# Performance work log

Hardware: AMD Instinct MI355X
Metric: run time of the kernel (lower is better)

Reference implementation:

```python
import jax, jax.numpy as jnp
import numpy as np
from functools import partial

MASK_THRESH = 0.4
SCORE_THRESH = 0.35
SUPPRESS_IOU = 0.85
TOPK_KEEP = 40


def _logit(p):
    p = jnp.clip(p, 1e-4, 1.0 - 1e-4)
    return jnp.log(p) - jnp.log1p(-p)


def _greedy_keep(binm_f, labels, scores):
    # binm_f: [N, HW] float 0/1 masks, rows already sorted by descending score.
    # Precompute the pairwise mask-IoU matrix once (batched, memory-bound),
    # then run the sequential greedy suppression over the small NxN matrix.
    N = binm_f.shape[0]
    inter = binm_f @ binm_f.T                              # [N, N]
    area = jnp.sum(binm_f, axis=1)
    union = jnp.maximum(area[:, None] + area[None, :] - inter, 1.0)
    iou = inter / union
    conflict = (labels[:, None] == labels[None, :]) & (iou >= SUPPRESS_IOU)

    def body(i, state):
        kept, count, stopped = state
        stopped = stopped | (scores[i] < SCORE_THRESH)     # break on low score
        clash = jnp.any(kept & conflict[i])                # same-class high-IoU vs kept
        take = (~stopped) & (~clash)
        kept = kept.at[i].set(take)
        count = count + take.astype(jnp.int32)
        stopped = stopped | (count >= TOPK_KEEP)           # break after topk kept
        return kept, count, stopped

    kept0 = jnp.zeros((N,), dtype=bool)
    kept, count, _ = jax.lax.fori_loop(0, N, body, (kept0, jnp.int32(0), jnp.array(False)))
    return kept, count


def _per_image(masks, labels, scores, feat, class_count):
    N, H, W = masks.shape
    D, fh, fw = feat.shape
    order = jnp.argsort(-scores)
    masks = masks[order]
    labels = labels[order]
    scores = scores[order]
    binm = masks > MASK_THRESH
    kept, count = _greedy_keep(binm.reshape(N, -1).astype(masks.dtype), labels, scores)

    # pack kept entries into the leading slots, preserving score order
    key = jnp.where(kept, jnp.arange(N), N + jnp.arange(N))
    perm = jnp.argsort(key)
    masks_p = jnp.clip(masks[perm], 0.0, 1.0)
    labels_p = jnp.clip(labels[perm], 0, class_count - 1)
    scores_p = jnp.clip(scores[perm], 0.0, 1.0)
    valid = jnp.arange(N) < count                          # [Q], Q == N == max_queries

    mask_logits = jnp.where(valid[:, None, None], _logit(masks_p), -20.0)

    C1 = class_count + 1
    base = jnp.full((N, C1), -10.0, dtype=masks.dtype)     # default row (all -10)
    row = base.at[:, -1].set(0.0)                          # no-object col -> 0
    onehot = jax.nn.one_hot(labels_p, C1, dtype=masks.dtype)
    row = row + onehot * (_logit(scores_p)[:, None] + 10.0)
    class_logits = jnp.where(valid[:, None], row, base)

    binm_p = masks_p > MASK_THRESH
    xs = jnp.arange(W, dtype=masks.dtype)
    ys = jnp.arange(H, dtype=masks.dtype)
    big = jnp.asarray(1e9, masks.dtype)
    x1 = jnp.min(jnp.where(binm_p, xs[None, None, :], big), axis=(1, 2))
    x2 = jnp.max(jnp.where(binm_p, xs[None, None, :], -big), axis=(1, 2))
    y1 = jnp.min(jnp.where(binm_p, ys[None, :, None], big), axis=(1, 2))
    y2 = jnp.max(jnp.where(binm_p, ys[None, :, None], -big), axis=(1, 2))
    cx = (x1 + x2) * 0.5 / W
    cy = (y1 + y2) * 0.5 / H
    bw = jnp.maximum(x2 - x1, 0.0) / W
    bh = jnp.maximum(y2 - y1, 0.0) / H
    box = jnp.clip(jnp.stack([cx, cy, bw, bh], axis=-1), 0.0, 1.0)
    has_px = jnp.any(binm_p, axis=(1, 2))
    boxes = jnp.where((valid & has_px)[:, None], box, 0.0)

    # mask-pooled DINO embeddings (bilinear downsample == F.interpolate align_corners=False)
    mask_small = jax.image.resize(masks_p, (N, fh, fw), method='linear')
    denom = jnp.maximum(jnp.sum(mask_small, axis=(1, 2)), 1e-6)
    pooled = jnp.einsum('qhw,dhw->qd', mask_small, feat) / denom[:, None]
    norm = jnp.maximum(jnp.linalg.norm(pooled, axis=-1, keepdims=True), 1e-12)
    embs = jnp.where(valid[:, None], pooled / norm, 0.0)
    return mask_logits, class_logits, boxes, embs


def reference(masks, labels, scores, dino_feat_map, class_count):
    fn = lambda m, l, s, f: _per_image(m, l, s, f, class_count)
    return jax.vmap(fn)(masks, labels, scores, dino_feat_map)


def setup_inputs():
    key = jax.random.key(0)
    k1, k2, k3, k4 = jax.random.split(key, 4)
    B, N, H, W = 2, 100, 640, 640
    D, fh, fw = 384, 40, 40
    return {
        'masks': jax.random.uniform(k1, (B, N, H, W), dtype=jnp.float32),
        'labels': jax.random.randint(k2, (B, N), 0, 80),
        'scores': jax.random.uniform(k3, (B, N), dtype=jnp.float32),
        'dino_feat_map': jax.random.normal(k4, (B, D, fh, fw), dtype=jnp.float32),
        'class_count': 80,
    }
```

## Files before the change

### kernel.cpp

```cpp
#include <hip/hip_runtime.h>
#include <cstdint>
#include <climits>

constexpr int kB = 2;
constexpr int kN = 100;
constexpr int kH = 640;
constexpr int kW = 640;
constexpr int kHW = kH * kW;
constexpr int kWORDS = kHW / 64;
constexpr int kD = 384;
constexpr int kFH = 40;
constexpr int kFW = 40;
constexpr int kC = 80;
constexpr int kC1 = kC + 1;
constexpr int kTOPK = 40;
constexpr int kCW = 2;

constexpr float MASK_THRESH = 0.4f;
constexpr float SCORE_THRESH = 0.35f;
constexpr float SUPPRESS_IOU = 0.85f;

constexpr size_t O_MASK = 0;
constexpr size_t O_CLS  = (size_t)kB * kN * kHW;
constexpr size_t O_BOX  = O_CLS + (size_t)kB * kN * kC1;
constexpr size_t O_EMB  = O_BOX + (size_t)kB * kN * 4;

__device__ __forceinline__ float logitf_(float p) {
    p = fminf(fmaxf(p, 1e-4f), 1.0f - 1e-4f);
    return logf(p) - log1pf(-p);
}

__global__ void k0_sort_init(const float* __restrict__ scores,
                             const int* __restrict__ labels,
                             int* __restrict__ order, float* __restrict__ sScore,
                             int* __restrict__ sLabel, int* __restrict__ area,
                             int* __restrict__ bbox,
                             unsigned long long* __restrict__ confRow,
                             float* __restrict__ denom) {
    int b = blockIdx.x;
    int t = threadIdx.x;
    __shared__ float s[kN];
    if (t < kN) s[t] = scores[b * kN + t];
    __syncthreads();
    if (t < kN) {
        float si = s[t];
        int rank = 0;
        for (int j = 0; j < kN; ++j) {
            float sj = s[j];
            if (sj > si || (sj == si && j < t)) rank++;
        }
        order[b * kN + rank]  = t;
        sScore[b * kN + rank] = si;
        sLabel[b * kN + rank] = labels[b * kN + t];
        area[b * kN + t] = 0;
        bbox[(b * kN + t) * 4 + 0] = INT_MAX;
        bbox[(b * kN + t) * 4 + 1] = INT_MIN;
        bbox[(b * kN + t) * 4 + 2] = INT_MAX;
        bbox[(b * kN + t) * 4 + 3] = INT_MIN;
        confRow[(b * kN + t) * kCW + 0] = 0ull;
        confRow[(b * kN + t) * kCW + 1] = 0ull;
        if (t < kTOPK) denom[b * kTOPK + t] = 0.0f;
    }
}

constexpr int kSPLIT = 8;
__global__ __launch_bounds__(256) void k1_pack(
    const float* __restrict__ masks, const int* __restrict__ order,
    const float* __restrict__ sScore, unsigned long long* __restrict__ packed,
    int* __restrict__ area, int* __restrict__ bbox) {
    int b = blockIdx.z, slot = blockIdx.y;
    if (sScore[b * kN + slot] < SCORE_THRESH) return;
    int q = order[b * kN + slot];
    const float4* src = (const float4*)(masks + (size_t)(b * kN + q) * kHW);
    unsigned long long* dst = packed + (size_t)(b * kN + slot) * (size_t)kWORDS;
    int lane = threadIdx.x & 63;
    int wv = threadIdx.x >> 6;
    const int wordsPerBlock = kWORDS / kSPLIT;
    const int wordsPerWave = wordsPerBlock / 4;
    int wbase = blockIdx.x * wordsPerBlock + wv * wordsPerWave;
    int pixBase = wbase * 64;

    int areaAcc = 0;
    int x1 = INT_MAX, x2 = INT_MIN, y1 = INT_MAX, y2 = INT_MIN;
#pragma unroll 2
    for (int i = 0; i < wordsPerWave / 4; ++i) {
        int pix = pixBase + i * 256 + lane * 4;
        float4 v = src[pix >> 2];
        bool p0 = v.x > MASK_THRESH, p1 = v.y > MASK_THRESH;
        bool p2 = v.z > MASK_THRESH, p3 = v.w > MASK_THRESH;
        unsigned long long b0 = __ballot(p0);
        unsigned long long b1 = __ballot(p1);
        unsigned long long b2 = __ballot(p2);
        unsigned long long b3 = __ballot(p3);
        if (lane == 0) {
            dst[wbase + 4 * i + 0] = b0;
            dst[wbase + 4 * i + 1] = b1;
            dst[wbase + 4 * i + 2] = b2;
            dst[wbase + 4 * i + 3] = b3;
        }
        int cnt = (int)p0 + (int)p1 + (int)p2 + (int)p3;
        areaAcc += cnt;
        if (cnt) {
            int row  = pix / kW;
            int col0 = pix - row * kW;
            int lo = p0 ? 0 : (p1 ? 1 : (p2 ? 2 : 3));
            int hi = p3 ? 3 : (p2 ? 2 : (p1 ? 1 : 0));
            x1 = min(x1, col0 + lo); x2 = max(x2, col0 + hi);
            y1 = min(y1, row);       y2 = max(y2, row);
        }
    }
#pragma unroll
    for (int off = 32; off > 0; off >>= 1) {
        areaAcc += __shfl_down(areaAcc, off);
        x1 = min(x1, __shfl_down(x1, off));
        x2 = max(x2, __shfl_down(x2, off));
        y1 = min(y1, __shfl_down(y1, off));
        y2 = max(y2, __shfl_down(y2, off));
    }
    __shared__ int sA[4], sx1[4], sx2[4], sy1[4], sy2[4];
    if (lane == 0) { sA[wv] = areaAcc; sx1[wv] = x1; sx2[wv] = x2; sy1[wv] = y1; sy2[wv] = y2; }
    __syncthreads();
    if (threadIdx.x == 0) {
        int A   = sA[0] + sA[1] + sA[2] + sA[3];
        int bx1 = min(min(sx1[0], sx1[1]), min(sx1[2], sx1[3]));
        int bx2 = max(max(sx2[0], sx2[1]), max(sx2[2], sx2[3]));
        int by1 = min(min(sy1[0], sy1[1]), min(sy1[2], sy1[3]));
        int by2 = max(max(sy2[0], sy2[1]), max(sy2[2], sy2[3]));
        if (A) atomicAdd(&area[b * kN + slot], A);
        if (bx1 != INT_MAX) {
            atomicMin(&bbox[(b * kN + slot) * 4 + 0], bx1);
            atomicMax(&bbox[(b * kN + slot) * 4 + 1], bx2);
            atomicMin(&bbox[(b * kN + slot) * 4 + 2], by1);
            atomicMax(&bbox[(b * kN + slot) * 4 + 3], by2);
        }
    }
}

__global__ __launch_bounds__(256) void k2a_conflict(
    const unsigned long long* __restrict__ packed,
    const int* __restrict__ sLabel, const float* __restrict__ sScore,
    const int* __restrict__ area, unsigned long long* __restrict__ confRow) {
    int i = blockIdx.x, j = blockIdx.y, b = blockIdx.z;
    if (j >= i) return;
    if (sScore[b * kN + i] < SCORE_THRESH) return;
    if (sLabel[b * kN + i] != sLabel[b * kN + j]) return;
    const unsigned long long* pi = packed + (size_t)(b * kN + i) * kWORDS;
    const unsigned long long* pj = packed + (size_t)(b * kN + j) * kWORDS;
    int acc = 0;
    for (int w = threadIdx.x; w < kWORDS; w += 256)
        acc += __popcll(pi[w] & pj[w]);
    __shared__ int s[256];
    s[threadIdx.x] = acc;
    __syncthreads();
    for (int st = 128; st > 0; st >>= 1) {
        if (threadIdx.x < st) s[threadIdx.x] += s[threadIdx.x + st];
        __syncthreads();
    }
    if (threadIdx.x == 0) {
        float inter = (float)s[0];
        float un = fmaxf((float)area[b * kN + i] + (float)area[b * kN + j] - inter, 1.0f);
        if (inter / un >= SUPPRESS_IOU)
            atomicOr(&confRow[(b * kN + i) * kCW + (j >> 6)], 1ull << (j & 63));
    }
}

__global__ __launch_bounds__(256) void k2b_greedy_clsbox(
    const float* __restrict__ sScore, const int* __restrict__ order,
    const unsigned long long* __restrict__ confRow,
    const int* __restrict__ sLabel, const int* __restrict__ area,
    const int* __restrict__ bbox, int* __restrict__ src_q,
    int* __restrict__ keep_s, int* __restrict__ countArr,
    float* __restrict__ out) {
    int b = blockIdx.x;
    int t = threadIdx.x;
    __shared__ float sc[kN];
    __shared__ int   ord[kN];
    __shared__ unsigned long long cr[kN * kCW];
    __shared__ int   ks[kN];
    __shared__ int   cnt_s;
    for (int e = t; e < kN; e += 256) {
        sc[e]  = sScore[b * kN + e];
        ord[e] = order[b * kN + e];
    }
    for (int e = t; e < kN * kCW; e += 256)
        cr[e] = confRow[(size_t)b * kN * kCW + e];
    __syncthreads();

    if (t == 0) {
        unsigned long long keptLo = 0ull, keptHi = 0ull;
        bool stopped = false;
        int count = 0;
        for (int i = 0; i < kN; ++i) {
            if (sc[i] < SCORE_THRESH) stopped = true;
            unsigned long long cl = cr[i * kCW + 0] & keptLo;
            unsigned long long ch = cr[i * kCW + 1] & keptHi;
            bool take = (!stopped) && ((cl | ch) == 0ull);
            if (take) {
                if (i < 64) keptLo |= 1ull << i; else keptHi |= 1ull << (i - 64);
                src_q[b * kN + count]  = ord[i];
                keep_s[b * kN + count] = i;
                ks[count] = i;
                count++;
                if (count >= kTOPK) stopped = true;
            }
        }
        countArr[b] = count;
        cnt_s = count;
        for (int s = count; s < kN; ++s) {
            src_q[b * kN + s] = -1; keep_s[b * kN + s] = -1; ks[s] = -1;
        }
    }
    __syncthreads();
    int count = cnt_s;

    for (int e = t; e < kN * kC1; e += 256) {
        int slot = e / kC1, c = e % kC1;
        float val = -10.0f;
        if (slot < count) {
            int s2 = ks[slot];
            int lab = min(max(sLabel[b * kN + s2], 0), kC - 1);
            float scv = fminf(fmaxf(sc[s2], 0.f), 1.f);
            if (c == lab) val = logitf_(scv);
            else if (c == kC1 - 1) val = 0.0f;
        }
        out[O_CLS + (size_t)b * kN * kC1 + e] = val;
    }
    for (int slot = t; slot < kN; slot += 256) {
        float bx[4] = {0.f, 0.f, 0.f, 0.f};
        if (slot < count) {
            int s2 = ks[slot];
            if (area[b * kN + s2] > 0) {
                float x1 = (float)bbox[(b * kN + s2) * 4 + 0];
                float x2 = (float)bbox[(b * kN + s2) * 4 + 1];
                float y1 = (float)bbox[(b * kN + s2) * 4 + 2];
                float y2 = (float)bbox[(b * kN + s2) * 4 + 3];
                bx[0] = fminf(fmaxf((x1 + x2) * 0.5f / kW, 0.f), 1.f);
                bx[1] = fminf(fmaxf((y1 + y2) * 0.5f / kH, 0.f), 1.f);
                bx[2] = fminf(fmaxf(fmaxf(x2 - x1, 0.f) / kW, 0.f), 1.f);
                bx[3] = fminf(fmaxf(fmaxf(y2 - y1, 0.f) / kH, 0.f), 1.f);
            }
        }
        for (int c4 = 0; c4 < 4; ++c4)
            out[O_BOX + (size_t)(b * kN + slot) * 4 + c4] = bx[c4];
    }
}

__global__ __launch_bounds__(256) void k3_logits_resizex(
    const float* __restrict__ masks, const int* __restrict__ src_q,
    float* __restrict__ out, float* __restrict__ S1) {
    int b = blockIdx.z, slot = blockIdx.y;
    int q = src_q[b * kN + slot];
    int lane = threadIdx.x & 63, wv = threadIdx.x >> 6;
    int y = blockIdx.x * 4 + wv;
    float4* dst = (float4*)(out + O_MASK + (size_t)(b * kN + slot) * kHW) + (size_t)y * 160;

    if (q < 0) {
        float4 f = make_float4(-20.f, -20.f, -20.f, -20.f);
        dst[lane] = f;
        dst[64 + lane] = f;
        if (lane < 32) dst[128 + lane] = f;
        return;
    }

    __shared__ float rbuf[4][660];
    const float4* src = (const float4*)(masks + (size_t)(b * kN + q) * kHW) + (size_t)y * 160;
#pragma unroll
    for (int i = 0; i < 3; ++i) {
        int idx = i * 64 + lane;
        if (idx < 160) {
            float4 m = src[idx];
            float4 o;
            o.x = logitf_(m.x); o.y = logitf_(m.y);
            o.z = logitf_(m.z); o.w = logitf_(m.w);
            dst[idx] = o;
            int col = idx * 4;
            int pad = col >> 5;
            rbuf[wv][col + pad + 0] = fminf(fmaxf(m.x, 0.f), 1.f);
            rbuf[wv][col + pad + 1] = fminf(fmaxf(m.y, 0.f), 1.f);
            rbuf[wv][col + pad + 2] = fminf(fmaxf(m.z, 0.f), 1.f);
            rbuf[wv][col + pad + 3] = fminf(fmaxf(m.w, 0.f), 1.f);
        }
    }
    __syncthreads();
    if (lane < kFW) {
        int ox = lane;
        float c = 16.0f * ox + 7.5f;
        float s = 0.f;
#pragma unroll
        for (int t = 0; t < 32; ++t) {
            int j = 16 * ox - 8 + t;
            if (j >= 0 && j < kW) {
                float w = 1.0f - fabsf((float)j - c) * (1.0f / 16.0f);
                s += w * rbuf[wv][j + (j >> 5)];
            }
        }
        float rs = (ox == 0 || ox == kFW - 1) ? (1.0f / 14.0f) : (1.0f / 16.0f);
        S1[((size_t)(b * kTOPK + slot) * kH + y) * kFW + ox] = s * rs;
    }
}

__global__ __launch_bounds__(256) void k6_resize_y(
    const float* __restrict__ S1, const int* __restrict__ countArr,
    float* __restrict__ msmall, float* __restrict__ denom) {
    int k = blockIdx.y, b = blockIdx.z;
    if (k >= countArr[b]) return;
    const float* src = S1 + (size_t)(b * kTOPK + k) * kH * kFW;
    int e0 = blockIdx.x * 320;
    float tot = 0.f;
    for (int ee = threadIdx.x; ee < 320; ee += 256) {
        int e = e0 + ee;
        int oy = e / kFW, ox = e % kFW;
        float c = 16.0f * oy + 7.5f;
        int j0 = max(0, 16 * oy - 8), j1 = min(kH - 1, 16 * oy + 23);
        float s = 0.f;
        for (int j = j0; j <= j1; ++j) {
            float w = 1.0f - fabsf((float)j - c) * (1.0f / 16.0f);
            s += w * src[(size_t)j * kFW + ox];
        }
        float rs = (oy == 0 || oy == kFH - 1) ? (1.0f / 14.0f) : (1.0f / 16.0f);
        s *= rs;
        msmall[(size_t)(b * kTOPK + k) * kFH * kFW + e] = s;
        tot += s;
    }
    __shared__ float sm[256];
    sm[threadIdx.x] = tot;
    __syncthreads();
    for (int st = 128; st > 0; st >>= 1) {
        if (threadIdx.x < st) sm[threadIdx.x] += sm[threadIdx.x + st];
        __syncthreads();
    }
    if (threadIdx.x == 0) atomicAdd(&denom[b * kTOPK + k], sm[0]);
}

__global__ __launch_bounds__(256) void k7_pool(
    const float* __restrict__ feat, const float* __restrict__ msmall,
    const float* __restrict__ denom, const int* __restrict__ countArr,
    float* __restrict__ pooled) {
    int d = blockIdx.x, b = blockIdx.y;
    int lane = threadIdx.x & 63, wv = threadIdx.x >> 6;
    const float* fp = feat + ((size_t)b * kD + d) * (kFH * kFW);
    float f[25];
#pragma unroll
    for (int i = 0; i < 25; ++i) f[i] = fp[i * 64 + lane];
    int count = countArr[b];
    for (int k = wv; k < count; k += 4) {
        const float* sp = msmall + (size_t)(b * kTOPK + k) * (kFH * kFW);
        float acc = 0.f;
#pragma unroll
        for (int i = 0; i < 25; ++i) acc += f[i] * sp[i * 64 + lane];
        for (int off = 32; off > 0; off >>= 1) acc += __shfl_down(acc, off);
        if (lane == 0)
            pooled[(size_t)(b * kTOPK + k) * kD + d] =
                acc / fmaxf(denom[b * kTOPK + k], 1e-6f);
    }
}

__global__ void k8_embs(const float* __restrict__ pooled,
                        const int* __restrict__ countArr,
                        float* __restrict__ out) {
    int slot = blockIdx.x, b = blockIdx.y;
    int count = countArr[b];
    float* dst = out + O_EMB + (size_t)(b * kN + slot) * kD;
    if (slot >= count) {
        for (int e = threadIdx.x; e < kD; e += 128) dst[e] = 0.f;
        return;
    }
    const float* p = pooled + (size_t)(b * kTOPK + slot) * kD;
    float ss = 0.f;
    for (int e = threadIdx.x; e < kD; e += 128) { float v = p[e]; ss += v * v; }
    __shared__ float sm[128];
    sm[threadIdx.x] = ss;
    __syncthreads();
    for (int st = 64; st > 0; st >>= 1) {
        if (threadIdx.x < st) sm[threadIdx.x] += sm[threadIdx.x + st];
        __syncthreads();
    }
    float norm = fmaxf(sqrtf(sm[0]), 1e-12f);
    for (int e = threadIdx.x; e < kD; e += 128) dst[e] = p[e] / norm;
}

extern "C" void kernel_launch(void* const* d_in, const int* in_sizes, int n_in,
                              void* d_out, int out_size, void* d_ws, size_t ws_size,
                              hipStream_t stream) {
    const float* masks  = (const float*)d_in[0];
    const int*   labels = (const int*)d_in[1];
    const float* scores = (const float*)d_in[2];
    const float* feat   = (const float*)d_in[3];
    float* out = (float*)d_out;

    char* ws = (char*)d_ws;
    auto take = [&](size_t bytes) { char* p = ws; ws += (bytes + 255) & ~(size_t)255; return p; };
    unsigned long long* packed = (unsigned long long*)take((size_t)kB * kN * kWORDS * 8);
    float* S1     = (float*)take((size_t)kB * kTOPK * kH * kFW * 4);
    float* msmall = (float*)take((size_t)kB * kTOPK * kFH * kFW * 4);
    float* pooled = (float*)take((size_t)kB * kTOPK * kD * 4);
    float* sScore = (float*)take((size_t)kB * kN * 4);
    float* denom  = (float*)take((size_t)kB * kTOPK * 4);
    int* order    = (int*)take((size_t)kB * kN * 4);
    int* sLabel   = (int*)take((size_t)kB * kN * 4);
    int* area     = (int*)take((size_t)kB * kN * 4);
    int* bbox     = (int*)take((size_t)kB * kN * 4 * 4);
    int* src_q    = (int*)take((size_t)kB * kN * 4);
    int* keep_s   = (int*)take((size_t)kB * kN * 4);
    int* countArr = (int*)take((size_t)kB * 4);
    unsigned long long* confRow = (unsigned long long*)take((size_t)kB * kN * kCW * 8);

    k0_sort_init<<<dim3(kB), dim3(128), 0, stream>>>(scores, labels, order, sScore,
                                                     sLabel, area, bbox, confRow, denom);
    k1_pack<<<dim3(kSPLIT, kN, kB), dim3(256), 0, stream>>>(masks, order, sScore,
                                                            packed, area, bbox);
    k2a_conflict<<<dim3(kN, kN, kB), dim3(256), 0, stream>>>(packed, sLabel, sScore,
                                                             area, confRow);
    k2b_greedy_clsbox<<<dim3(kB), dim3(256), 0, stream>>>(sScore, order, confRow,
                                                          sLabel, area, bbox, src_q,
                                                          keep_s, countArr, out);
    k3_logits_resizex<<<dim3(kH / 4, kN, kB), dim3(256), 0, stream>>>(masks, src_q,
                                                                      out, S1);
    k6_resize_y<<<dim3(5, kTOPK, kB), dim3(256), 0, stream>>>(S1, countArr, msmall,
                                                              denom);
    k7_pool<<<dim3(kD, kB), dim3(256), 0, stream>>>(feat, msmall, denom, countArr,
                                                    pooled);
    k8_embs<<<dim3(kN, kB), dim3(128), 0, stream>>>(pooled, countArr, out);
}
```

Before: 691.1 us.

## Compact conflict pairs, use fast logit, nontemporal stores, split padded-slot fill

The sort kernel now builds a compact list of same-label, above-threshold pairs, so the conflict kernel runs a fixed grid over only those pairs instead of launching N*N*B mostly idle blocks. The logit uses a fast log2 and divide in place of logf/log1pf. Mask output writes switch to nontemporal stores. The logits kernel launches only TOPK slots, and a separate fill kernel writes the -20 padding for the remaining slots. The fast logit may differ slightly in precision from the exact version.

```diff
diff --git a/kernel.cpp b/kernel.cpp
--- a/kernel.cpp
+++ b/kernel.cpp
@@ -15,6 +15,7 @@
 constexpr int kC1 = kC + 1;
 constexpr int kTOPK = 40;
 constexpr int kCW = 2;
+constexpr int kPairMax = kN * (kN - 1) / 2;
 
 constexpr float MASK_THRESH = 0.4f;
 constexpr float SCORE_THRESH = 0.35f;
@@ -25,9 +26,21 @@
 constexpr size_t O_BOX  = O_CLS + (size_t)kB * kN * kC1;
 constexpr size_t O_EMB  = O_BOX + (size_t)kB * kN * 4;
 
+typedef float floatx4 __attribute__((ext_vector_type(4)));
+__device__ __forceinline__ void nt_store4(const float4& v, float4* p) {
+    floatx4 t; t.x = v.x; t.y = v.y; t.z = v.z; t.w = v.w;
+    __builtin_nontemporal_store(t, (floatx4*)p);
+}
+
 __device__ __forceinline__ float logitf_(float p) {
     p = fminf(fmaxf(p, 1e-4f), 1.0f - 1e-4f);
     return logf(p) - log1pf(-p);
+}
+
+__device__ __forceinline__ float logit_fast(float p) {
+    p = fminf(fmaxf(p, 1e-4f), 1.0f - 1e-4f);
+    float r = __fdividef(p, 1.0f - p);
+    return __log2f(r) * 0.69314718056f;
 }
 
 __global__ void k0_sort_init(const float* __restrict__ scores,
@@ -36,11 +49,17 @@
                              int* __restrict__ sLabel, int* __restrict__ area,
                              int* __restrict__ bbox,
                              unsigned long long* __restrict__ confRow,
-                             float* __restrict__ denom) {
+                             float* __restrict__ denom,
+                             int* __restrict__ pairList,
+                             int* __restrict__ pairCount) {
     int b = blockIdx.x;
     int t = threadIdx.x;
     __shared__ float s[kN];
-    if (t < kN) s[t] = scores[b * kN + t];
+    __shared__ int   lb[kN];
+    __shared__ float ssort[kN];
+    __shared__ int   lsort[kN];
+    if (t < kN) { s[t] = scores[b * kN + t]; lb[t] = labels[b * kN + t]; }
+    if (t == 0) pairCount[b] = 0;
     __syncthreads();
     if (t < kN) {
         float si = s[t];
@@ -51,7 +70,9 @@
         }
         order[b * kN + rank]  = t;
         sScore[b * kN + rank] = si;
-        sLabel[b * kN + rank] = labels[b * kN + t];
+        sLabel[b * kN + rank] = lb[t];
+        ssort[rank] = si;
+        lsort[rank] = lb[t];
         area[b * kN + t] = 0;
         bbox[(b * kN + t) * 4 + 0] = INT_MAX;
         bbox[(b * kN + t) * 4 + 1] = INT_MIN;
@@ -60,6 +81,14 @@
         confRow[(b * kN + t) * kCW + 0] = 0ull;
         confRow[(b * kN + t) * kCW + 1] = 0ull;
         if (t < kTOPK) denom[b * kTOPK + t] = 0.0f;
+    }
+    __syncthreads();
+    for (int idx = t; idx < kN * kN; idx += 128) {
+        int i = idx / kN, j = idx - i * kN;
+        if (j < i && lsort[i] == lsort[j] && ssort[i] >= SCORE_THRESH) {
+            int pos = atomicAdd(&pairCount[b], 1);
+            pairList[b * kPairMax + pos] = (i << 16) | j;
+        }
     }
 }
 
@@ -138,29 +167,32 @@
 
 __global__ __launch_bounds__(256) void k2a_conflict(
     const unsigned long long* __restrict__ packed,
-    const int* __restrict__ sLabel, const float* __restrict__ sScore,
-    const int* __restrict__ area, unsigned long long* __restrict__ confRow) {
-    int i = blockIdx.x, j = blockIdx.y, b = blockIdx.z;
-    if (j >= i) return;
-    if (sScore[b * kN + i] < SCORE_THRESH) return;
-    if (sLabel[b * kN + i] != sLabel[b * kN + j]) return;
-    const unsigned long long* pi = packed + (size_t)(b * kN + i) * kWORDS;
-    const unsigned long long* pj = packed + (size_t)(b * kN + j) * kWORDS;
-    int acc = 0;
-    for (int w = threadIdx.x; w < kWORDS; w += 256)
-        acc += __popcll(pi[w] & pj[w]);
+    const int* __restrict__ area, const int* __restrict__ pairList,
+    const int* __restrict__ pairCount, unsigned long long* __restrict__ confRow) {
+    int b = blockIdx.y;
+    int np = pairCount[b];
     __shared__ int s[256];
-    s[threadIdx.x] = acc;
-    __syncthreads();
-    for (int st = 128; st > 0; st >>= 1) {
-        if (threadIdx.x < st) s[threadIdx.x] += s[threadIdx.x + st];
+    for (int p = blockIdx.x; p < np; p += gridDim.x) {
+        int pr = pairList[b * kPairMax + p];
+        int i = pr >> 16, j = pr & 0xffff;
+        const unsigned long long* pi = packed + (size_t)(b * kN + i) * kWORDS;
+        const unsigned long long* pj = packed + (size_t)(b * kN + j) * kWORDS;
+        int acc = 0;
+        for (int w = threadIdx.x; w < kWORDS; w += 256)
+            acc += __popcll(pi[w] & pj[w]);
+        s[threadIdx.x] = acc;
         __syncthreads();
-    }
-    if (threadIdx.x == 0) {
-        float inter = (float)s[0];
-        float un = fmaxf((float)area[b * kN + i] + (float)area[b * kN + j] - inter, 1.0f);
-        if (inter / un >= SUPPRESS_IOU)
-            atomicOr(&confRow[(b * kN + i) * kCW + (j >> 6)], 1ull << (j & 63));
+        for (int st = 128; st > 0; st >>= 1) {
+            if (threadIdx.x < st) s[threadIdx.x] += s[threadIdx.x + st];
+            __syncthreads();
+        }
+        if (threadIdx.x == 0) {
+            float inter = (float)s[0];
+            float un = fmaxf((float)area[b * kN + i] + (float)area[b * kN + j] - inter, 1.0f);
+            if (inter / un >= SUPPRESS_IOU)
+                atomicOr(&confRow[(b * kN + i) * kCW + (j >> 6)], 1ull << (j & 63));
+        }
+        __syncthreads();
     }
 }
 
@@ -256,9 +288,9 @@
 
     if (q < 0) {
         float4 f = make_float4(-20.f, -20.f, -20.f, -20.f);
-        dst[lane] = f;
-        dst[64 + lane] = f;
-        if (lane < 32) dst[128 + lane] = f;
+        nt_store4(f, dst + lane);
+        nt_store4(f, dst + 64 + lane);
+        if (lane < 32) nt_store4(f, dst + 128 + lane);
         return;
     }
 
@@ -270,9 +302,9 @@
         if (idx < 160) {
             float4 m = src[idx];
             float4 o;
-            o.x = logitf_(m.x); o.y = logitf_(m.y);
-            o.z = logitf_(m.z); o.w = logitf_(m.w);
-            dst[idx] = o;
+            o.x = logit_fast(m.x); o.y = logit_fast(m.y);
+            o.z = logit_fast(m.z); o.w = logit_fast(m.w);
+            nt_store4(o, dst + idx);
             int col = idx * 4;
             int pad = col >> 5;
             rbuf[wv][col + pad + 0] = fminf(fmaxf(m.x, 0.f), 1.f);
@@ -297,6 +329,16 @@
         float rs = (ox == 0 || ox == kFW - 1) ? (1.0f / 14.0f) : (1.0f / 16.0f);
         S1[((size_t)(b * kTOPK + slot) * kH + y) * kFW + ox] = s * rs;
     }
+}
+
+__global__ __launch_bounds__(256) void k3f_fill(float* __restrict__ out) {
+    int b = blockIdx.y;
+    float4* base = (float4*)(out + O_MASK + ((size_t)b * kN + kTOPK) * (size_t)kHW);
+    const size_t n4 = (size_t)(kN - kTOPK) * kHW / 4;
+    float4 f = make_float4(-20.f, -20.f, -20.f, -20.f);
+    for (size_t i = (size_t)blockIdx.x * 256 + threadIdx.x; i < n4;
+         i += (size_t)gridDim.x * 256)
+        nt_store4(f, base + i);
 }
 
 __global__ __launch_bounds__(256) void k6_resize_y(
@@ -404,18 +446,22 @@
     int* keep_s   = (int*)take((size_t)kB * kN * 4);
     int* countArr = (int*)take((size_t)kB * 4);
     unsigned long long* confRow = (unsigned long long*)take((size_t)kB * kN * kCW * 8);
+    int* pairList  = (int*)take((size_t)kB * kPairMax * 4);
+    int* pairCount = (int*)take((size_t)kB * 4);
 
     k0_sort_init<<<dim3(kB), dim3(128), 0, stream>>>(scores, labels, order, sScore,
-                                                     sLabel, area, bbox, confRow, denom);
+                                                     sLabel, area, bbox, confRow,
+                                                     denom, pairList, pairCount);
     k1_pack<<<dim3(kSPLIT, kN, kB), dim3(256), 0, stream>>>(masks, order, sScore,
                                                             packed, area, bbox);
-    k2a_conflict<<<dim3(kN, kN, kB), dim3(256), 0, stream>>>(packed, sLabel, sScore,
-                                                             area, confRow);
+    k2a_conflict<<<dim3(512, kB), dim3(256), 0, stream>>>(packed, area, pairList,
+                                                          pairCount, confRow);
     k2b_greedy_clsbox<<<dim3(kB), dim3(256), 0, stream>>>(sScore, order, confRow,
                                                           sLabel, area, bbox, src_q,
                                                           keep_s, countArr, out);
-    k3_logits_resizex<<<dim3(kH / 4, kN, kB), dim3(256), 0, stream>>>(masks, src_q,
-                                                                      out, S1);
+    k3_logits_resizex<<<dim3(kH / 4, kTOPK, kB), dim3(256), 0, stream>>>(masks, src_q,
+                                                                         out, S1);
+    k3f_fill<<<dim3(1024, kB), dim3(256), 0, stream>>>(out);
     k6_resize_y<<<dim3(5, kTOPK, kB), dim3(256), 0, stream>>>(S1, countArr, msmall,
                                                               denom);
     k7_pool<<<dim3(kD, kB), dim3(256), 0, stream>>>(feat, msmall, denom, countArr,
```

New measurement: 628.9 us. 1.1x faster.
